# Optimization experiments

Measured on AMD Instinct MI355X. Metric: run time of the kernel, lower is better.

Reference implementation:

```python
import jax, jax.numpy as jnp
import numpy as np

N = 50000
E = 1600000
D_IN = 128
D_HID = 128
K = 16  # n_clusters


def spmm(edge_index, edge_weight, feats):
    # out[i] = sum_{(i<-j) in edges} w_e * feats[j]
    dst, src = edge_index[0], edge_index[1]
    msgs = feats[src] * edge_weight[:, None]  # [E, d]
    return jax.ops.segment_sum(msgs, dst, num_segments=N)


def gcn_with_skip(x, edge_index, edge_weight, W, b, skip_w):
    transformed = x @ W + b                      # Linear kernel
    propagated = spmm(edge_index, edge_weight, transformed)
    return jax.nn.selu(skip_w * transformed + propagated)


def setup_inputs() -> dict:
    key = jax.random.key(0)
    ks = jax.random.split(key, 12)
    x = jax.random.normal(ks[0], (N, D_IN), dtype=jnp.float32)
    edge_index = jax.random.randint(ks[1], (2, E), 0, N, dtype=jnp.int32)
    edge_weight = jax.random.uniform(ks[2], (E,), dtype=jnp.float32)
    s1 = 1.0 / np.sqrt(D_IN)
    s2 = 1.0 / np.sqrt(D_HID)
    W1 = jax.random.uniform(ks[3], (D_IN, D_HID), jnp.float32, -s1, s1)
    b1 = jax.random.uniform(ks[4], (D_HID,), jnp.float32, -s1, s1)
    skip1 = jnp.ones((D_HID,), jnp.float32)
    W2 = jax.random.uniform(ks[5], (D_HID, D_HID), jnp.float32, -s2, s2)
    b2 = jax.random.uniform(ks[6], (D_HID,), jnp.float32, -s2, s2)
    skip2 = jnp.ones((D_HID,), jnp.float32)
    Wa = jax.random.uniform(ks[7], (D_HID, K), jnp.float32, -s2, s2)
    ba = jax.random.uniform(ks[8], (K,), jnp.float32, -s2, s2)
    return {"x": x, "edge_index": edge_index, "edge_weight": edge_weight,
            "W1": W1, "b1": b1, "skip1": skip1,
            "W2": W2, "b2": b2, "skip2": skip2,
            "Wa": Wa, "ba": ba}


def reference(x, edge_index, edge_weight, W1, b1, skip1, W2, b2, skip2, Wa, ba):
    h = gcn_with_skip(x, edge_index, edge_weight, W1, b1, skip1)
    h = gcn_with_skip(h, edge_index, edge_weight, W2, b2, skip2)
    assignments = jax.nn.softmax(h @ Wa + ba, axis=-1)  # [N, K]
    return assignments
```

## Files before the change

### kernel.cpp

```cpp
#include <hip/hip_runtime.h>
#include <hip/hip_bf16.h>
#include <hip/hip_fp16.h>

#define NN 50000
#define NE 1600000
#define DD 128
#define KC 16

#define NB 3125
#define CHUNK 5120
#define NCHUNK 313
#define BT 1024
#define EPT 5
#define MAXB 768
#define SB 772

#define G1B 98
#define ZBLK 13
#define HB_LD 136

typedef __attribute__((ext_vector_type(8))) short s8v;
typedef __attribute__((ext_vector_type(4))) float f4v;
typedef __attribute__((ext_vector_type(2))) float f2v;

#define FMIXW_LO(a, wf, pk) \
    asm("v_fma_mix_f32 %0, %1, %2, %0 op_sel:[0,0,0] op_sel_hi:[0,1,0]" \
        : "+v"(a) : "v"(wf), "v"(pk))
#define FMIXW_HI(a, wf, pk) \
    asm("v_fma_mix_f32 %0, %1, %2, %0 op_sel:[0,1,0] op_sel_hi:[0,1,0]" \
        : "+v"(a) : "v"(wf), "v"(pk))

__device__ __forceinline__ f2v uph2(unsigned u) {
    __half2 h = *reinterpret_cast<__half2*>(&u);
    f2v r;
    r.x = __low2float(h);
    r.y = __high2float(h);
    return r;
}


__device__ __forceinline__ void wprep_one(const float* __restrict__ W, s8v* __restrict__ Wf, int g) {
    int l = g & 63;
    int kcnt = g >> 6;
    int kc = kcnt >> 3, nt = kcnt & 7;
    int n = nt * 16 + (l & 15);
    int kb = kc * 32 + (l >> 4) * 8;
    union { s8v v; __hip_bfloat162 h2[4]; } u;
    #pragma unroll
    for (int q = 0; q < 4; q++) {
        float lo = W[(size_t)(kb + 2 * q) * 128 + n];
        float hi = W[(size_t)(kb + 2 * q + 1) * 128 + n];
        u.h2[q] = __float22bfloat162_rn(make_float2(lo, hi));
    }
    Wf[(size_t)kcnt * 64 + l] = u.v;
}


__global__ __launch_bounds__(256) void k_init(int* __restrict__ gcur,
                                              const float* __restrict__ W1,
                                              const float* __restrict__ W2,
                                              s8v* __restrict__ Wf1,
                                              s8v* __restrict__ Wf2) {
    int bid = blockIdx.x, t = threadIdx.x;
    if (bid < ZBLK) {
        int i = bid * 256 + t;
        if (i < NB) gcur[i] = 0;
        return;
    }
    int wb = bid - ZBLK;
    if (wb < 8) wprep_one(W1, Wf1, wb * 256 + t);
    else        wprep_one(W2, Wf2, (wb - 8) * 256 + t);
}


__device__ __forceinline__ s8v load_afrag(const float* p) {
    union { s8v v; __hip_bfloat162 h2[4]; } a;
    float4 f0 = *(const float4*)p;
    float4 f1 = *(const float4*)(p + 4);
    a.h2[0] = __float22bfloat162_rn(make_float2(f0.x, f0.y));
    a.h2[1] = __float22bfloat162_rn(make_float2(f0.z, f0.w));
    a.h2[2] = __float22bfloat162_rn(make_float2(f1.x, f1.y));
    a.h2[3] = __float22bfloat162_rn(make_float2(f1.z, f1.w));
    return a.v;
}

__device__ __forceinline__ void gemm_body(const float* __restrict__ X,
                                          const s8v* __restrict__ Wf,
                                          const float* __restrict__ bias,
                                          __half* __restrict__ Out,
                                          int nrows, int wave, int lane) {
    int m0 = wave * 32;
    if (m0 >= nrows) return;
    int col = lane & 15;
    int quad = lane >> 4;

    f4v acc[2][8];
    #pragma unroll
    for (int mt = 0; mt < 2; mt++)
        #pragma unroll
        for (int nt = 0; nt < 8; nt++) acc[mt][nt] = (f4v){0.f, 0.f, 0.f, 0.f};

    int row0 = m0 + col;
    int row1 = m0 + 16 + col;
    if (row0 >= nrows) row0 = nrows - 1;
    if (row1 >= nrows) row1 = nrows - 1;
    const float* xr0 = X + (size_t)row0 * 128 + quad * 8;
    const float* xr1 = X + (size_t)row1 * 128 + quad * 8;

    #pragma unroll 1
    for (int kc = 0; kc < 4; kc++) {
        s8v a0 = load_afrag(xr0 + kc * 32);
        s8v a1 = load_afrag(xr1 + kc * 32);
        #pragma unroll
        for (int nt = 0; nt < 8; nt++) {
            s8v b = Wf[(size_t)(kc * 8 + nt) * 64 + lane];
            acc[0][nt] = __builtin_amdgcn_mfma_f32_16x16x32_bf16(a0, b, acc[0][nt], 0, 0, 0);
            acc[1][nt] = __builtin_amdgcn_mfma_f32_16x16x32_bf16(a1, b, acc[1][nt], 0, 0, 0);
        }
    }

    float bb[8];
    #pragma unroll
    for (int nt = 0; nt < 8; nt++) bb[nt] = bias[nt * 16 + col];

    #pragma unroll
    for (int mt = 0; mt < 2; mt++) {
        #pragma unroll
        for (int r = 0; r < 4; r++) {
            int row = m0 + mt * 16 + quad * 4 + r;
            if (row < nrows) {
                __half* orow = Out + (size_t)row * 128 + col;
                #pragma unroll
                for (int nt = 0; nt < 8; nt++) {
                    orow[nt * 16] = __float2half(acc[mt][nt][r] + bb[nt]);
                }
            }
        }
    }
}


__global__ __launch_bounds__(BT) void k_binprep(const int* __restrict__ dst,
                                                const int* __restrict__ src,
                                                const float* __restrict__ w,
                                                int2* __restrict__ staging,
                                                int* __restrict__ gcur,
                                                const float* __restrict__ x,
                                                const s8v* __restrict__ Wf1,
                                                const float* __restrict__ b1,
                                                __half* __restrict__ T) {
    __shared__ int cnt[NB];
    __shared__ int s[BT];
    __shared__ int2 lrec[CHUNK];
    int t = threadIdx.x;
    int bid = blockIdx.x;

    if (bid >= NCHUNK) {
        int wave = (bid - NCHUNK) * 16 + (t >> 6);
        gemm_body(x, Wf1, b1, T, NN, wave, t & 63);
        return;
    }

    int c = bid;
    size_t cbase = (size_t)c * CHUNK;
    for (int i = t; i < NB; i += BT) cnt[i] = 0;
    __syncthreads();

    int dreg[EPT], sreg[EPT]; float wreg[EPT];
    #pragma unroll
    for (int j = 0; j < EPT; j++) {
        size_t e = cbase + j * BT + t;
        bool ok = e < NE;
        size_t ee = ok ? e : (NE - 1);
        dreg[j] = dst[ee]; sreg[j] = src[ee]; wreg[j] = w[ee];
        if (!ok) dreg[j] = -1;
        if (ok) atomicAdd(&cnt[dreg[j] >> 4], 1);
    }
    __syncthreads();

    int v[4]; int sum = 0;
    #pragma unroll
    for (int j = 0; j < 4; j++) { int i = t * 4 + j; v[j] = (i < NB) ? cnt[i] : 0; sum += v[j]; }
    s[t] = sum; __syncthreads();
    for (int off = 1; off < BT; off <<= 1) {
        int u = (t >= off) ? s[t - off] : 0;
        __syncthreads();
        s[t] += u;
        __syncthreads();
    }
    int run = (t == 0) ? 0 : s[t - 1];
    int st4[4];
    #pragma unroll
    for (int j = 0; j < 4; j++) {
        int i = t * 4 + j;
        st4[j] = run;
        if (i < NB) { cnt[i] = run; run += v[j]; }
    }
    __syncthreads();

    #pragma unroll
    for (int j = 0; j < EPT; j++) {
        if (dreg[j] >= 0) {
            int b = dreg[j] >> 4;
            int li = atomicAdd(&cnt[b], 1);
            lrec[li] = make_int2(sreg[j] | ((dreg[j] & 15) << 16), __float_as_int(wreg[j]));
        }
    }
    __syncthreads();

    #pragma unroll
    for (int j = 0; j < 4; j++) {
        int i = t * 4 + j;
        if (i < NB && v[j] > 0) {
            int gb = atomicAdd(&gcur[i], v[j]);
            int2* dp = staging + (size_t)i * SB;
            for (int k = 0; k < v[j]; k++) {
                int p = gb + k;
                if (p < MAXB) dp[p] = lrec[st4[j] + k];
            }
        }
    }
}


template <int MODE>
__global__ __launch_bounds__(256) void k_spmm(const __half* __restrict__ T,
                                              const int2* __restrict__ staging,
                                              const int* __restrict__ gcur,
                                              const float* __restrict__ skip,
                                              const s8v* __restrict__ Wfb,
                                              const float* __restrict__ bias2,
                                              __half* __restrict__ T2,
                                              const float* __restrict__ Wa,
                                              const float* __restrict__ ba,
                                              float* __restrict__ aout) {
    __shared__ __align__(16) int2 srec[MAXB + 8];
    __shared__ int rcnt[16];
    __shared__ int rowoff[17];
    __shared__ __align__(16) __hip_bfloat16 hbuf[(MODE == 0) ? (16 * HB_LD) : 8];
    int b = blockIdx.x;
    int tid = threadIdx.x;
    int wv = tid >> 6, lane = tid & 63;
    int q = lane >> 4;
    int fk = lane & 15;

    int cnt = gcur[b];
    if (cnt > MAXB) cnt = MAXB;

    if (tid < 16) rcnt[tid] = 0;
    __syncthreads();

    const int2* gp = staging + (size_t)b * SB;
    int i0 = tid, i1 = tid + 256, i2 = tid + 512;
    bool h0 = i0 < cnt, h1 = i1 < cnt, h2 = i2 < cnt;
    int2 mr0, mr1, mr2;
    if (h0) { mr0 = gp[i0]; atomicAdd(&rcnt[(unsigned)mr0.x >> 16], 1); }
    if (h1) { mr1 = gp[i1]; atomicAdd(&rcnt[(unsigned)mr1.x >> 16], 1); }
    if (h2) { mr2 = gp[i2]; atomicAdd(&rcnt[(unsigned)mr2.x >> 16], 1); }
    __syncthreads();

    if (tid < 16) {
        int vv = rcnt[tid];
        int p = vv;
        #pragma unroll
        for (int off = 1; off < 16; off <<= 1) {
            int u = __shfl_up(p, off, 64);
            if (tid >= off) p += u;
        }
        rowoff[tid] = p - vv;
        if (tid == 15) rowoff[16] = p;
        rcnt[tid] = p - vv;
    }
    __syncthreads();

    if (h0) { int p = atomicAdd(&rcnt[(unsigned)mr0.x >> 16], 1); srec[p] = mr0; }
    if (h1) { int p = atomicAdd(&rcnt[(unsigned)mr1.x >> 16], 1); srec[p] = mr1; }
    if (h2) { int p = atomicAdd(&rcnt[(unsigned)mr2.x >> 16], 1); srec[p] = mr2; }
    if (tid < 8) srec[cnt + tid] = make_int2(0, 0);
    __syncthreads();

    const char* Tb = (const char*)T;
    unsigned foff = (unsigned)fk << 4;

    float sk[8];
    *(float4*)&sk[0] = *(const float4*)(skip + fk * 8);
    *(float4*)&sk[4] = *(const float4*)(skip + fk * 8 + 4);

    float wreg[32];
    float bav[4];
    if (MODE == 1) {
        #pragma unroll
        for (int j = 0; j < 8; j++)
            *(float4*)&wreg[j * 4] = *(const float4*)(Wa + (size_t)(8 * fk + j) * KC + 4 * q);
        #pragma unroll
        for (int c = 0; c < 4; c++) bav[c] = ba[4 * q + c];
    }

    const float scale = 1.0507009873554805f, alpha = 1.6732632423543772f;

    for (int r = wv; r < 16; r += 4) {
        int g = b * 16 + r;
        int o = rowoff[r], oe = rowoff[r + 1];
        float ac[8];
        #pragma unroll
        for (int j = 0; j < 8; j++) ac[j] = 0.f;

        #define LDT(rc) (*(const int4*)(Tb + (((unsigned)(rc).x & 0xFFFFu) * 256u + foff)))
        #define EDGE(rc, t4)                                               \
            do {                                                           \
                float wf_ = __int_as_float((rc).y);                        \
                FMIXW_LO(ac[0], wf_, (t4).x); FMIXW_HI(ac[1], wf_, (t4).x);\
                FMIXW_LO(ac[2], wf_, (t4).y); FMIXW_HI(ac[3], wf_, (t4).y);\
                FMIXW_LO(ac[4], wf_, (t4).z); FMIXW_HI(ac[5], wf_, (t4).z);\
                FMIXW_LO(ac[6], wf_, (t4).w); FMIXW_HI(ac[7], wf_, (t4).w);\
            } while (0)

        for (; o + 32 <= oe; o += 32) {
            int2 r0 = srec[o + q],      r1 = srec[o + 4 + q];
            int2 r2 = srec[o + 8 + q],  r3 = srec[o + 12 + q];
            int2 r4 = srec[o + 16 + q], r5 = srec[o + 20 + q];
            int2 r6 = srec[o + 24 + q], r7 = srec[o + 28 + q];
            int4 t0 = LDT(r0); int4 t1 = LDT(r1); int4 t2 = LDT(r2); int4 t3 = LDT(r3);
            int4 t4 = LDT(r4); int4 t5 = LDT(r5); int4 t6 = LDT(r6); int4 t7 = LDT(r7);
            EDGE(r0, t0); EDGE(r1, t1); EDGE(r2, t2); EDGE(r3, t3);
            EDGE(r4, t4); EDGE(r5, t5); EDGE(r6, t6); EDGE(r7, t7);
        }
        for (; o + 16 <= oe; o += 16) {
            int2 r0 = srec[o + q],     r1 = srec[o + 4 + q];
            int2 r2 = srec[o + 8 + q], r3 = srec[o + 12 + q];
            int4 t0 = LDT(r0); int4 t1 = LDT(r1); int4 t2 = LDT(r2); int4 t3 = LDT(r3);
            EDGE(r0, t0); EDGE(r1, t1); EDGE(r2, t2); EDGE(r3, t3);
        }
        for (; o + 8 <= oe; o += 8) {
            int2 r0 = srec[o + q], r1 = srec[o + 4 + q];
            int4 t0 = LDT(r0); int4 t1 = LDT(r1);
            EDGE(r0, t0); EDGE(r1, t1);
        }
        for (; o < oe; o += 4) {
            int i = o + q;
            int2 r0 = (i < oe) ? srec[i] : make_int2(0, 0);
            int4 t0 = LDT(r0);
            EDGE(r0, t0);
        }
        #undef EDGE
        #undef LDT

        #pragma unroll
        for (int j = 0; j < 8; j++) {
            ac[j] += __shfl_xor(ac[j], 16, 64);
            ac[j] += __shfl_xor(ac[j], 32, 64);
        }

        int4 ts = *(const int4*)(Tb + ((unsigned)g * 256u + foff));
        f2v s01 = uph2(ts.x), s23 = uph2(ts.y), s45 = uph2(ts.z), s67 = uph2(ts.w);
        float v[8];
        v[0] = sk[0] * s01.x + ac[0]; v[1] = sk[1] * s01.y + ac[1];
        v[2] = sk[2] * s23.x + ac[2]; v[3] = sk[3] * s23.y + ac[3];
        v[4] = sk[4] * s45.x + ac[4]; v[5] = sk[5] * s45.y + ac[5];
        v[6] = sk[6] * s67.x + ac[6]; v[7] = sk[7] * s67.y + ac[7];
        #pragma unroll
        for (int j = 0; j < 8; j++)
            v[j] = scale * (v[j] > 0.f ? v[j] : alpha * (__expf(v[j]) - 1.f));

        if (MODE == 0) {
            if (q == 0) {
                union { int4 i4; __hip_bfloat162 h2[4]; } pk;
                #pragma unroll
                for (int j = 0; j < 4; j++)
                    pk.h2[j] = __float22bfloat162_rn(make_float2(v[2 * j], v[2 * j + 1]));
                *(int4*)&hbuf[r * HB_LD + fk * 8] = pk.i4;
            }
        } else {
            float p4[4] = {0.f, 0.f, 0.f, 0.f};
            #pragma unroll
            for (int j = 0; j < 8; j++)
                #pragma unroll
                for (int c = 0; c < 4; c++) p4[c] += v[j] * wreg[j * 4 + c];
            #pragma unroll
            for (int off = 1; off <= 8; off <<= 1)
                #pragma unroll
                for (int c = 0; c < 4; c++) p4[c] += __shfl_xor(p4[c], off, 64);
            #pragma unroll
            for (int c = 0; c < 4; c++) p4[c] += bav[c];
            float m = fmaxf(fmaxf(p4[0], p4[1]), fmaxf(p4[2], p4[3]));
            m = fmaxf(m, __shfl_xor(m, 16, 64));
            m = fmaxf(m, __shfl_xor(m, 32, 64));
            float e0 = __expf(p4[0] - m), e1 = __expf(p4[1] - m);
            float e2 = __expf(p4[2] - m), e3 = __expf(p4[3] - m);
            float s = e0 + e1 + e2 + e3;
            s += __shfl_xor(s, 16, 64);
            s += __shfl_xor(s, 32, 64);
            if (fk < 4) {
                float ev = e0;
                ev = (fk == 1) ? e1 : ev;
                ev = (fk == 2) ? e2 : ev;
                ev = (fk == 3) ? e3 : ev;
                aout[(size_t)g * KC + 4 * q + fk] = ev / s;
            }
        }
    }

    if (MODE == 0) {
        __syncthreads();
        int col = fk;
        int quad = q;
        int nt0 = wv * 2, nt1 = nt0 + 1;
        f4v acc0 = (f4v){0.f, 0.f, 0.f, 0.f};
        f4v acc1 = (f4v){0.f, 0.f, 0.f, 0.f};
        #pragma unroll
        for (int kc = 0; kc < 4; kc++) {
            s8v a = *(const s8v*)&hbuf[col * HB_LD + kc * 32 + quad * 8];
            s8v b0 = Wfb[(size_t)(kc * 8 + nt0) * 64 + lane];
            s8v b1 = Wfb[(size_t)(kc * 8 + nt1) * 64 + lane];
            acc0 = __builtin_amdgcn_mfma_f32_16x16x32_bf16(a, b0, acc0, 0, 0, 0);
            acc1 = __builtin_amdgcn_mfma_f32_16x16x32_bf16(a, b1, acc1, 0, 0, 0);
        }
        float bb0 = bias2[nt0 * 16 + col];
        float bb1 = bias2[nt1 * 16 + col];
        #pragma unroll
        for (int r4 = 0; r4 < 4; r4++) {
            int grow = b * 16 + quad * 4 + r4;
            __half* orow = T2 + (size_t)grow * 128;
            orow[nt0 * 16 + col] = __float2half(acc0[r4] + bb0);
            orow[nt1 * 16 + col] = __float2half(acc1[r4] + bb1);
        }
    }
}


extern "C" void kernel_launch(void* const* d_in, const int* in_sizes, int n_in,
                              void* d_out, int out_size, void* d_ws, size_t ws_size,
                              hipStream_t stream) {
    const float* x     = (const float*)d_in[0];
    const int*   eidx  = (const int*)d_in[1];
    const float* ew    = (const float*)d_in[2];
    const float* W1    = (const float*)d_in[3];
    const float* b1    = (const float*)d_in[4];
    const float* skip1 = (const float*)d_in[5];
    const float* W2    = (const float*)d_in[6];
    const float* b2    = (const float*)d_in[7];
    const float* skip2 = (const float*)d_in[8];
    const float* Wa    = (const float*)d_in[9];
    const float* ba    = (const float*)d_in[10];
    float* out = (float*)d_out;

    const int* dst = eidx;
    const int* src = eidx + NE;

    char* ws = (char*)d_ws;
    size_t off = 0;
    __half* T  = (__half*)(ws + off);                 off += (size_t)NN * DD * 2;
    __half* T2 = (__half*)(ws + off);                 off += (size_t)NN * DD * 2;
    int2* staging = (int2*)(ws + off);                off += (size_t)NB * SB * 8;
    int* gcur = (int*)(ws + off);                     off += (size_t)NB * 4 + 1024;
    s8v* Wf1 = (s8v*)(ws + off);                      off += 2048 * 16;
    s8v* Wf2 = (s8v*)(ws + off);                      off += 2048 * 16;

    k_init<<<ZBLK + 16, 256, 0, stream>>>(gcur, W1, W2, Wf1, Wf2);
    k_binprep<<<NCHUNK + G1B, BT, 0, stream>>>(dst, src, ew, staging, gcur,
                                               x, Wf1, b1, T);
    k_spmm<0><<<NB, 256, 0, stream>>>(T, staging, gcur, skip1,
                                      Wf2, b2, T2, nullptr, nullptr, nullptr);
    k_spmm<1><<<NB, 256, 0, stream>>>(T2, staging, gcur, skip2,
                                      nullptr, nullptr, nullptr, Wa, ba, out);
}
```

Baseline: 278.2 us.

## Replace block-local scan binning with direct global-offset scatter into bucket staging

The edge-binning kernel drops the block-wide prefix scan and the local shared-memory record buffer. Each block now reserves global bucket offsets with one atomic per nonzero bucket count, then scatters each edge record straight to its staging slot using a shared atomic cursor. Block size, chunk size and edges-per-thread are retuned (512 threads, 12 edges each), and the GEMM wave mapping and block count are adjusted to match. This removes many barriers and the serial per-bucket copy loop, at the cost of scattered, uncoalesced global writes.

```diff
diff --git a/kernel.cpp b/kernel.cpp
--- a/kernel.cpp
+++ b/kernel.cpp
@@ -8,14 +8,14 @@
 #define KC 16
 
 #define NB 3125
-#define CHUNK 5120
-#define NCHUNK 313
-#define BT 1024
-#define EPT 5
+#define CHUNK 6144
+#define NCHUNK 261
+#define BT 512
+#define EPT 12
 #define MAXB 768
 #define SB 772
 
-#define G1B 98
+#define G1B 196
 #define ZBLK 13
 #define HB_LD 136
 
@@ -150,13 +150,11 @@
                                                 const float* __restrict__ b1,
                                                 __half* __restrict__ T) {
     __shared__ int cnt[NB];
-    __shared__ int s[BT];
-    __shared__ int2 lrec[CHUNK];
     int t = threadIdx.x;
     int bid = blockIdx.x;
 
     if (bid >= NCHUNK) {
-        int wave = (bid - NCHUNK) * 16 + (t >> 6);
+        int wave = (bid - NCHUNK) * 8 + (t >> 6);
         gemm_body(x, Wf1, b1, T, NN, wave, t & 63);
         return;
     }
@@ -178,23 +176,9 @@
     }
     __syncthreads();
 
-    int v[4]; int sum = 0;
-    #pragma unroll
-    for (int j = 0; j < 4; j++) { int i = t * 4 + j; v[j] = (i < NB) ? cnt[i] : 0; sum += v[j]; }
-    s[t] = sum; __syncthreads();
-    for (int off = 1; off < BT; off <<= 1) {
-        int u = (t >= off) ? s[t - off] : 0;
-        __syncthreads();
-        s[t] += u;
-        __syncthreads();
-    }
-    int run = (t == 0) ? 0 : s[t - 1];
-    int st4[4];
-    #pragma unroll
-    for (int j = 0; j < 4; j++) {
-        int i = t * 4 + j;
-        st4[j] = run;
-        if (i < NB) { cnt[i] = run; run += v[j]; }
+    for (int i = t; i < NB; i += BT) {
+        int cc = cnt[i];
+        if (cc > 0) cnt[i] = atomicAdd(&gcur[i], cc);
     }
     __syncthreads();
 
@@ -202,22 +186,10 @@
     for (int j = 0; j < EPT; j++) {
         if (dreg[j] >= 0) {
             int b = dreg[j] >> 4;
-            int li = atomicAdd(&cnt[b], 1);
-            lrec[li] = make_int2(sreg[j] | ((dreg[j] & 15) << 16), __float_as_int(wreg[j]));
-        }
-    }
-    __syncthreads();
-
-    #pragma unroll
-    for (int j = 0; j < 4; j++) {
-        int i = t * 4 + j;
-        if (i < NB && v[j] > 0) {
-            int gb = atomicAdd(&gcur[i], v[j]);
-            int2* dp = staging + (size_t)i * SB;
-            for (int k = 0; k < v[j]; k++) {
-                int p = gb + k;
-                if (p < MAXB) dp[p] = lrec[st4[j] + k];
-            }
+            int pos = atomicAdd(&cnt[b], 1);
+            if (pos < MAXB)
+                staging[(size_t)b * SB + pos] =
+                    make_int2(sreg[j] | ((dreg[j] & 15) << 16), __float_as_int(wreg[j]));
         }
     }
 }
```

Result: faster. 243.8 us (-12.4%).
